# Kernel optimization log

Measured on AMD Instinct MI355X. Metric: run time of the kernel, lower is better.

## Reference

```python
import jax, jax.numpy as jnp
import numpy as np

N_NODES = 100000
N_EDGES = 1600000
D_FEAT = 256
UNITS = 128


def setup_inputs() -> dict:
    key = jax.random.key(0)
    k1, k2, k3, k4, k5 = jax.random.split(key, 5)
    x = jax.random.normal(k1, (N_NODES, D_FEAT), dtype=jnp.float32)
    # glorot-scale init for w (scale doesn't affect correctness checking)
    w = jax.random.normal(k2, (D_FEAT, UNITS), dtype=jnp.float32) * (2.0 / (D_FEAT + UNITS)) ** 0.5
    adj_src = jax.random.randint(k3, (N_EDGES,), 0, N_NODES, dtype=jnp.int64)
    adj_dst = jax.random.randint(k4, (N_EDGES,), 0, N_NODES, dtype=jnp.int64)
    adj_vals = jax.random.uniform(k5, (N_EDGES,), dtype=jnp.float32)
    return {"x": x, "w": w, "adj_src": adj_src, "adj_dst": adj_dst, "adj_vals": adj_vals}


def reference(x, w, adj_src, adj_dst, adj_vals):
    # x: [N, D], w: [D, U]  -> dense projection
    h = x @ w  # [N, U]
    # sparse_dense_matmul(adj_norm, h): out[i] = sum_j A[i,j] * h[j]
    # COO: edge e contributes adj_vals[e] * h[adj_src[e]] to row adj_dst[e]
    msgs = adj_vals[:, None] * h[adj_src]  # [E, U]
    out = jax.ops.segment_sum(msgs, adj_dst, num_segments=N_NODES)  # [N, U]
    return out
```

## Files before the change

kernel.cpp:

```cpp
#include <hip/hip_runtime.h>

#define D_FEAT 256
#define UNITS  128

#define NBITS  5
#define BINSZ  32
#define BINCAP 1024
#define MAXNB  3136

typedef __attribute__((ext_vector_type(8))) short short8;
typedef __attribute__((ext_vector_type(4))) float floatx4;

__device__ inline ushort f2bf(float f) {
    uint u = __float_as_uint(f);
    uint r = u + 0x7FFF + ((u >> 16) & 1);
    return (ushort)(r >> 16);
}

constexpr int WT_STRIDE = 264;

__global__ __launch_bounds__(256) void gemm_mfma_kernel(const float* __restrict__ x,
                                                        const float* __restrict__ w,
                                                        ushort* __restrict__ hb, int M) {
    __shared__ ushort wT[128 * WT_STRIDE];

    const int tid  = threadIdx.x;
    const int wave = tid >> 6;
    const int lane = tid & 63;
    const int quad = lane >> 4;
    const int m16  = lane & 15;

    const int row  = blockIdx.x * 64 + wave * 16 + m16;
    const int rowc = row < M ? row : M - 1;
    const float* xr = x + (size_t)rowc * D_FEAT;

    short8 afrag[8];
    #pragma unroll
    for (int s = 0; s < 8; ++s) {
        const float4* p = (const float4*)(xr + s * 32 + quad * 8);
        float4 lo = p[0];
        float4 hi = p[1];
        union { short8 v; ushort u[8]; } af;
        af.u[0] = f2bf(lo.x); af.u[1] = f2bf(lo.y);
        af.u[2] = f2bf(lo.z); af.u[3] = f2bf(lo.w);
        af.u[4] = f2bf(hi.x); af.u[5] = f2bf(hi.y);
        af.u[6] = f2bf(hi.z); af.u[7] = f2bf(hi.w);
        afrag[s] = af.v;
    }

    for (int f2 = tid; f2 < 128 * 128; f2 += 256) {
        int n  = f2 & 127;
        int kp = f2 >> 7;
        float w0 = w[(size_t)(2 * kp) * UNITS + n];
        float w1 = w[(size_t)(2 * kp + 1) * UNITS + n];
        uint p = (uint)f2bf(w0) | ((uint)f2bf(w1) << 16);
        *(uint*)&wT[n * WT_STRIDE + 2 * kp] = p;
    }
    __syncthreads();

    floatx4 acc[8] = {};
    #pragma unroll
    for (int s = 0; s < 8; ++s) {
        #pragma unroll
        for (int c = 0; c < 8; ++c) {
            short8 bfrag = *(const short8*)&wT[(c * 16 + m16) * WT_STRIDE + s * 32 + quad * 8];
            acc[c] = __builtin_amdgcn_mfma_f32_16x16x32_bf16(afrag[s], bfrag, acc[c], 0, 0, 0);
        }
    }

    #pragma unroll
    for (int c = 0; c < 8; ++c) {
        #pragma unroll
        for (int i = 0; i < 4; ++i) {
            int r = blockIdx.x * 64 + wave * 16 + quad * 4 + i;
            if (r < M) hb[(size_t)r * UNITS + c * 16 + m16] = f2bf(acc[c][i]);
        }
    }
}

__global__ __launch_bounds__(256) void coarse_scatter_kernel(const int* __restrict__ src,
                                                             const int* __restrict__ dst,
                                                             const float* __restrict__ vals,
                                                             int* __restrict__ cursor,
                                                             int2* __restrict__ staged,
                                                             int E, int NB, int chunk) {
    __shared__ int s_hist[MAXNB];
    __shared__ int s_base[MAXNB];

    const int tid = threadIdx.x;
    const int e0 = blockIdx.x * chunk;
    const int e1 = min(E, e0 + chunk);

    for (int i = tid; i < NB; i += 256) s_hist[i] = 0;
    __syncthreads();

    for (int e = e0 + tid; e < e1; e += 256)
        atomicAdd(&s_hist[dst[e] >> NBITS], 1);
    __syncthreads();

    for (int b = tid; b < NB; b += 256) {
        int c = s_hist[b];
        s_base[b] = (c > 0) ? atomicAdd(&cursor[b * 4], c) : 0;
    }
    __syncthreads();
    for (int i = tid; i < NB; i += 256) s_hist[i] = 0;
    __syncthreads();

    for (int e = e0 + tid; e < e1; e += 256) {
        int d = dst[e];
        int b = d >> NBITS;
        int r = s_base[b] + atomicAdd(&s_hist[b], 1);
        if (r < BINCAP) {
            int meta = src[e] | ((d & (BINSZ - 1)) << 20);
            staged[(size_t)b * BINCAP + r] = make_int2(meta, __float_as_int(vals[e]));
        }
    }
}

__global__ __launch_bounds__(256) void gather_sort_kernel(const int* __restrict__ cursor,
                                                          const int2* __restrict__ staged,
                                                          const ushort* __restrict__ hb,
                                                          float* __restrict__ out, int N) {
    __shared__ int2   ebuf[BINCAP];
    __shared__ ushort ids[BINCAP];
    __shared__ int cnt[BINSZ], ofs[BINSZ], cur[BINSZ];

    const int b   = blockIdx.x;
    const int tid = threadIdx.x;

    int n = cursor[b * 4];
    if (n > BINCAP) n = BINCAP;

    if (tid < BINSZ) cnt[tid] = 0;
    __syncthreads();

    const int2* sg = staged + (size_t)b * BINCAP;
    for (int i = tid; i < n; i += 256) {
        int2 e = sg[i];
        ebuf[i] = e;
        atomicAdd(&cnt[(e.x >> 20) & (BINSZ - 1)], 1);
    }
    __syncthreads();

    if (tid == 0) {
        int run = 0;
        #pragma unroll
        for (int d = 0; d < BINSZ; ++d) { ofs[d] = run; cur[d] = run; run += cnt[d]; }
    }
    __syncthreads();

    for (int i = tid; i < n; i += 256) {
        int dl = (ebuf[i].x >> 20) & (BINSZ - 1);
        int pos = atomicAdd(&cur[dl], 1);
        ids[pos] = (ushort)i;
    }
    __syncthreads();

    const int half = tid >> 5;
    const int lane = tid & 31;

    #pragma unroll
    for (int d0 = 0; d0 < BINSZ; d0 += 8) {
        int d  = d0 + half;
        int dg = b * BINSZ + d;
        if (dg >= N) continue;
        int start = ofs[d];
        int c     = cnt[d];

        float a0 = 0.f, a1 = 0.f, a2 = 0.f, a3 = 0.f;
        for (int j = 0; j < c; ++j) {
            int id = ids[start + j];
            int2 e = ebuf[id];
            float v = __int_as_float(e.y);
            int   s = e.x & 0xFFFFF;
            uint2 hv = *(const uint2*)(hb + (size_t)s * UNITS + lane * 4);
            a0 += v * __uint_as_float(hv.x << 16);
            a1 += v * __uint_as_float(hv.x & 0xFFFF0000u);
            a2 += v * __uint_as_float(hv.y << 16);
            a3 += v * __uint_as_float(hv.y & 0xFFFF0000u);
        }
        float4 r = make_float4(a0, a1, a2, a3);
        *(float4*)(out + (size_t)dg * UNITS + lane * 4) = r;
    }
}

extern "C" void kernel_launch(void* const* d_in, const int* in_sizes, int n_in,
                              void* d_out, int out_size, void* d_ws, size_t ws_size,
                              hipStream_t stream) {
    const float* x        = (const float*)d_in[0];
    const float* w        = (const float*)d_in[1];
    const int*   adj_src  = (const int*)d_in[2];
    const int*   adj_dst  = (const int*)d_in[3];
    const float* adj_vals = (const float*)d_in[4];
    float*       out      = (float*)d_out;

    const int M = in_sizes[0] / D_FEAT;
    const int E = in_sizes[2];
    const int NB = (M + BINSZ - 1) >> NBITS;

    char*   ws  = (char*)d_ws;
    ushort* hb  = (ushort*)ws;
    size_t  off = (size_t)M * UNITS * sizeof(ushort);
    off = (off + 15) & ~(size_t)15;
    int*    cursor = (int*)(ws + off);
    off += (size_t)NB * 4 * sizeof(int);
    off = (off + 15) & ~(size_t)15;
    int2*   staged = (int2*)(ws + off);

    hipMemsetAsync(cursor, 0, (size_t)NB * 4 * sizeof(int), stream);

    gemm_mfma_kernel<<<(M + 63) / 64, 256, 0, stream>>>(x, w, hb, M);

    const int chunk = (E + 255) / 256;
    coarse_scatter_kernel<<<256, 256, 0, stream>>>(adj_src, adj_dst, adj_vals,
                                                   cursor, staged, E, NB, chunk);

    gather_sort_kernel<<<NB, 256, 0, stream>>>(cursor, staged, hb, out, M);
}
```

Measured before the change: 330.5 us.

## Precompute bf16 transposed weights once, sort edge records directly, halve scatter blocks

A separate small kernel now converts and transposes w to bf16 a single time. Before, every GEMM block rebuilt this table in LDS, so the GEMM now reads B fragments straight from global memory/L2 with no shared-memory staging or barrier. The gather kernel sorts the full edge records into a second LDS buffer instead of a ushort index array, which removes one indirection per edge. The scatter launch drops from 256 to 128 blocks, cutting global cursor atomics but also lowering parallelism. The risk is that uncached global B-fragment loads in the GEMM may cost more than the LDS reads they replace.

```diff
diff --git a/kernel.cpp b/kernel.cpp
--- a/kernel.cpp
+++ b/kernel.cpp
@@ -17,13 +17,17 @@
     return (ushort)(r >> 16);
 }
 
-constexpr int WT_STRIDE = 264;
-
-__global__ __launch_bounds__(256) void gemm_mfma_kernel(const float* __restrict__ x,
-                                                        const float* __restrict__ w,
-                                                        ushort* __restrict__ hb, int M) {
-    __shared__ ushort wT[128 * WT_STRIDE];
-
+__global__ __launch_bounds__(256) void wt_prep_kernel(const float* __restrict__ w,
+                                                      ushort* __restrict__ wT) {
+    int idx = blockIdx.x * 256 + threadIdx.x;
+    int n = idx >> 8;
+    int k = idx & 255;
+    wT[n * 256 + k] = f2bf(w[(size_t)k * UNITS + n]);
+}
+
+__global__ __launch_bounds__(256) void gemm_mfma2_kernel(const float* __restrict__ x,
+                                                         const ushort* __restrict__ wT,
+                                                         ushort* __restrict__ hb, int M) {
     const int tid  = threadIdx.x;
     const int wave = tid >> 6;
     const int lane = tid & 63;
@@ -48,22 +52,12 @@
         afrag[s] = af.v;
     }
 
-    for (int f2 = tid; f2 < 128 * 128; f2 += 256) {
-        int n  = f2 & 127;
-        int kp = f2 >> 7;
-        float w0 = w[(size_t)(2 * kp) * UNITS + n];
-        float w1 = w[(size_t)(2 * kp + 1) * UNITS + n];
-        uint p = (uint)f2bf(w0) | ((uint)f2bf(w1) << 16);
-        *(uint*)&wT[n * WT_STRIDE + 2 * kp] = p;
-    }
-    __syncthreads();
-
     floatx4 acc[8] = {};
     #pragma unroll
     for (int s = 0; s < 8; ++s) {
         #pragma unroll
         for (int c = 0; c < 8; ++c) {
-            short8 bfrag = *(const short8*)&wT[(c * 16 + m16) * WT_STRIDE + s * 32 + quad * 8];
+            short8 bfrag = *(const short8*)&wT[(c * 16 + m16) * 256 + s * 32 + quad * 8];
             acc[c] = __builtin_amdgcn_mfma_f32_16x16x32_bf16(afrag[s], bfrag, acc[c], 0, 0, 0);
         }
     }
@@ -121,8 +115,8 @@
                                                           const int2* __restrict__ staged,
                                                           const ushort* __restrict__ hb,
                                                           float* __restrict__ out, int N) {
-    __shared__ int2   ebuf[BINCAP];
-    __shared__ ushort ids[BINCAP];
+    __shared__ int2 ebuf[BINCAP];
+    __shared__ int2 sbuf[BINCAP];
     __shared__ int cnt[BINSZ], ofs[BINSZ], cur[BINSZ];
 
     const int b   = blockIdx.x;
@@ -150,9 +144,10 @@
     __syncthreads();
 
     for (int i = tid; i < n; i += 256) {
-        int dl = (ebuf[i].x >> 20) & (BINSZ - 1);
+        int2 e = ebuf[i];
+        int dl = (e.x >> 20) & (BINSZ - 1);
         int pos = atomicAdd(&cur[dl], 1);
-        ids[pos] = (ushort)i;
+        sbuf[pos] = e;
     }
     __syncthreads();
 
@@ -169,8 +164,7 @@
 
         float a0 = 0.f, a1 = 0.f, a2 = 0.f, a3 = 0.f;
         for (int j = 0; j < c; ++j) {
-            int id = ids[start + j];
-            int2 e = ebuf[id];
+            int2 e = sbuf[start + j];
             float v = __int_as_float(e.y);
             int   s = e.x & 0xFFFFF;
             uint2 hv = *(const uint2*)(hb + (size_t)s * UNITS + lane * 4);
@@ -201,7 +195,9 @@
     char*   ws  = (char*)d_ws;
     ushort* hb  = (ushort*)ws;
     size_t  off = (size_t)M * UNITS * sizeof(ushort);
-    off = (off + 15) & ~(size_t)15;
+    off = (off + 255) & ~(size_t)255;
+    ushort* wT  = (ushort*)(ws + off);
+    off += (size_t)128 * 256 * sizeof(ushort);
     int*    cursor = (int*)(ws + off);
     off += (size_t)NB * 4 * sizeof(int);
     off = (off + 15) & ~(size_t)15;
@@ -209,11 +205,14 @@
 
     hipMemsetAsync(cursor, 0, (size_t)NB * 4 * sizeof(int), stream);
 
-    gemm_mfma_kernel<<<(M + 63) / 64, 256, 0, stream>>>(x, w, hb, M);
-
-    const int chunk = (E + 255) / 256;
-    coarse_scatter_kernel<<<256, 256, 0, stream>>>(adj_src, adj_dst, adj_vals,
-                                                   cursor, staged, E, NB, chunk);
+    wt_prep_kernel<<<128, 256, 0, stream>>>(w, wT);
+
+    gemm_mfma2_kernel<<<(M + 63) / 64, 256, 0, stream>>>(x, wT, hb, M);
+
+    const int NSCAT = 128;
+    const int chunk = (E + NSCAT - 1) / NSCAT;
+    coarse_scatter_kernel<<<NSCAT, 256, 0, stream>>>(adj_src, adj_dst, adj_vals,
+                                                     cursor, staged, E, NB, chunk);
 
     gather_sort_kernel<<<NB, 256, 0, stream>>>(cursor, staged, hb, out, M);
 }
```

After: 363.1 us. +9.9%, slower.
